# Optimization experiments

Hardware: AMD Instinct MI355X
Metric: run time of the kernel (lower is better)

The kernel has to match this reference:

```python
import jax, jax.numpy as jnp
import numpy as np

HEAD_DIM = 64
N_HEADS = 12
N_KV_HEADS = 4
N_REP = N_HEADS // N_KV_HEADS  # 3


def _rope(x, cos, sin):
    # x: [B, S, H, D]; cos/sin: [1, S, D//2] -> broadcast over heads
    x2 = x.reshape(*x.shape[:-1], -1, 2)          # [B,S,H,D/2,2]
    x_r, x_i = x2[..., 0], x2[..., 1]
    c = cos[:, :, None, :]                         # [1,S,1,D/2]
    s = sin[:, :, None, :]
    o_r = x_r * c - x_i * s
    o_i = x_r * s + x_i * c
    return jnp.stack([o_r, o_i], axis=-1).reshape(x.shape)


def setup_inputs() -> dict:
    key = jax.random.key(0)
    ks = jax.random.split(key, 6)
    B, S, H = 4, 2048, 768
    hidden_state = jax.random.normal(ks[0], (B, S, H), dtype=jnp.float32)
    # true RoPE frequencies (theta=10000) for positions 0..S-1
    inv_freq = 1.0 / (10000.0 ** (np.arange(0, HEAD_DIM, 2, dtype=np.float32) / HEAD_DIM))
    ang = np.arange(S, dtype=np.float32)[:, None] * inv_freq[None, :]  # [S, D/2]
    freqs_cos = jnp.asarray(np.cos(ang))[None]     # [1,S,32]
    freqs_sin = jnp.asarray(np.sin(ang))[None]
    sc = 0.02
    wq = jax.random.normal(ks[1], (768, 768), dtype=jnp.float32) * sc
    wk = jax.random.normal(ks[2], (256, 768), dtype=jnp.float32) * sc
    wv = jax.random.normal(ks[3], (256, 768), dtype=jnp.float32) * sc
    wo = jax.random.normal(ks[4], (768, 768), dtype=jnp.float32) * sc
    return {"hidden_state": hidden_state, "freqs_cos": freqs_cos, "freqs_sin": freqs_sin,
            "wq": wq, "wk": wk, "wv": wv, "wo": wo}


def reference(hidden_state, freqs_cos, freqs_sin, wq, wk, wv, wo):
    B, S, _ = hidden_state.shape
    q = (hidden_state @ wq.T).reshape(B, S, N_HEADS, HEAD_DIM)
    k = (hidden_state @ wk.T).reshape(B, S, N_KV_HEADS, HEAD_DIM)
    v = (hidden_state @ wv.T).reshape(B, S, N_KV_HEADS, HEAD_DIM)
    q = _rope(q, freqs_cos, freqs_sin)
    k = _rope(k, freqs_cos, freqs_sin)
    # repeat_kv: [B,S,KV,D] -> [B,S,KV*n_rep,D]
    k = jnp.repeat(k, N_REP, axis=2)
    v = jnp.repeat(v, N_REP, axis=2)
    q = q.transpose(0, 2, 1, 3)  # [B,H,S,D]
    k = k.transpose(0, 2, 1, 3)
    v = v.transpose(0, 2, 1, 3)
    scores = jnp.einsum('bhqd,bhkd->bhqk', q, k) / np.sqrt(HEAD_DIM).astype(np.float32)
    mask = jnp.triu(jnp.full((S, S), -jnp.inf, dtype=scores.dtype), k=1)
    scores = scores + mask
    attn = jax.nn.softmax(scores.astype(jnp.float32), axis=-1).astype(q.dtype)
    # dropout is inference-off (identity)
    out = jnp.einsum('bhqk,bhkd->bhqd', attn, v)
    out = out.transpose(0, 2, 1, 3).reshape(B, S, N_HEADS * HEAD_DIM)
    return out @ wo.T, attn
```

## Files before the change

kernel.cpp:

```cpp
#include <hip/hip_runtime.h>
#include <hip/hip_bf16.h>
#include <stdint.h>


typedef __bf16 bf16x8 __attribute__((ext_vector_type(8)));
typedef float  f32x4  __attribute__((ext_vector_type(4)));

#define B_    4
#define S_    2048
#define H_    768
#define NH_Q  12
#define NKV_  4
#define D_    64
#define MROWS (B_ * S_)
#define NQKV  1280
#define TILE_E (128 * 32)

__device__ __forceinline__ f32x4 mfma16(bf16x8 a, bf16x8 b, f32x4 c) {
  return __builtin_amdgcn_mfma_f32_16x16x32_bf16(a, b, c, 0, 0, 0);
}

__device__ __forceinline__ void st_nt4(float* p, f32x4 v) {
  __builtin_nontemporal_store(v, (f32x4*)p);
}

__device__ __forceinline__ uint32_t pk2(float a, float b) {
  __bf16 x = (__bf16)a, y = (__bf16)b;
  uint16_t xu = __builtin_bit_cast(uint16_t, x);
  uint16_t yu = __builtin_bit_cast(uint16_t, y);
  return (uint32_t)xu | ((uint32_t)yu << 16);
}
__device__ __forceinline__ float bl(uint32_t u) {
  uint32_t t = u << 16; return __builtin_bit_cast(float, t);
}
__device__ __forceinline__ float bh(uint32_t u) {
  uint32_t t = u & 0xffff0000u; return __builtin_bit_cast(float, t);
}

__device__ __forceinline__ void gload_lds16(const __bf16* g, __bf16* l) {
  __builtin_amdgcn_global_load_lds(
      (const __attribute__((address_space(1))) void*)g,
      (__attribute__((address_space(3))) void*)l, 16, 0, 0);
}

__global__ void cast_all(const float* __restrict__ X, const float* __restrict__ wq,
                         const float* __restrict__ wo, const float* __restrict__ wk,
                         const float* __restrict__ wv,
                         __bf16* __restrict__ Xb, __bf16* __restrict__ wqb,
                         __bf16* __restrict__ wob, __bf16* __restrict__ wkb,
                         __bf16* __restrict__ wvb) {
  int i = blockIdx.x * 256 + threadIdx.x;
  const int nX = MROWS * 768 / 8;
  const int nW = 768 * 768 / 8;
  const int nK = 256 * 768 / 8;
  const float* s; __bf16* d; int off;
  if (i < nX)                    { s = X;  d = Xb;  off = i; }
  else if (i < nX + nW)          { s = wq; d = wqb; off = i - nX; }
  else if (i < nX + 2 * nW)      { s = wo; d = wob; off = i - nX - nW; }
  else if (i < nX + 2 * nW + nK) { s = wk; d = wkb; off = i - nX - 2 * nW; }
  else if (i < nX + 2 * nW + 2 * nK) { s = wv; d = wvb; off = i - nX - 2 * nW - nK; }
  else return;
  const float4* sp = (const float4*)s + (size_t)off * 2;
  float4 a = sp[0], b = sp[1];
  bf16x8 o;
  o[0] = (__bf16)a.x; o[1] = (__bf16)a.y; o[2] = (__bf16)a.z; o[3] = (__bf16)a.w;
  o[4] = (__bf16)b.x; o[5] = (__bf16)b.y; o[6] = (__bf16)b.z; o[7] = (__bf16)b.w;
  *((bf16x8*)d + off) = o;
}

struct GemmPtrs {
  const __bf16 *gA0, *gA1, *gB0, *gB1;
};

__device__ __forceinline__ GemmPtrs make_ptrs(const __bf16* A, const __bf16* W,
                                              int m0, int n0, int K, int tid) {
  GemmPtrs gp;
  int c0 = tid, c1 = 256 + tid;
  int sr0 = c0 >> 2, kc0 = (c0 & 3) ^ ((sr0 >> 1) & 3);
  int sr1 = c1 >> 2, kc1 = (c1 & 3) ^ ((sr1 >> 1) & 3);
  gp.gA0 = A + (size_t)(m0 + sr0) * K + kc0 * 8;
  gp.gA1 = A + (size_t)(m0 + sr1) * K + kc1 * 8;
  gp.gB0 = W + (size_t)(n0 + sr0) * K + kc0 * 8;
  gp.gB1 = W + (size_t)(n0 + sr1) * K + kc1 * 8;
  return gp;
}

__device__ __forceinline__ void gemm_stage(GemmPtrs gp, int k0,
                                           __bf16* As, __bf16* Bs, int tid) {
  __bf16* lA0 = As + (size_t)(tid & ~63) * 8;
  __bf16* lB0 = Bs + (size_t)(tid & ~63) * 8;
  gload_lds16(gp.gA0 + k0, lA0);
  gload_lds16(gp.gA1 + k0, lA0 + 256 * 8);
  gload_lds16(gp.gB0 + k0, lB0);
  gload_lds16(gp.gB1 + k0, lB0 + 256 * 8);
}

__device__ __forceinline__ void gemm_core(GemmPtrs gp, int K,
                                          __bf16* As, __bf16* Bs,
                                          int tid, f32x4 (*acc)[4]) {
  const int lane = tid & 63, w = tid >> 6;
  const int wm = w >> 1, wn = w & 1;
  const int ql = lane & 15, grp = lane >> 4;

  gemm_stage(gp, 0, As, Bs, tid);
  __syncthreads();

  const int nk = K / 32;
  for (int ks = 0; ks < nk; ks++) {
    __bf16* curA = As + (ks & 1) * TILE_E;
    __bf16* curB = Bs + (ks & 1) * TILE_E;
    if (ks + 1 < nk)
      gemm_stage(gp, (ks + 1) * 32, As + ((ks + 1) & 1) * TILE_E,
                 Bs + ((ks + 1) & 1) * TILE_E, tid);

    bf16x8 af[4], bf_[4];
#pragma unroll
    for (int i = 0; i < 4; i++) {
      int row = wm * 64 + i * 16 + ql;
      int kc = grp ^ ((row >> 1) & 3);
      af[i] = *(const bf16x8*)(curA + row * 32 + kc * 8);
    }
#pragma unroll
    for (int j = 0; j < 4; j++) {
      int row = wn * 64 + j * 16 + ql;
      int kc = grp ^ ((row >> 1) & 3);
      bf_[j] = *(const bf16x8*)(curB + row * 32 + kc * 8);
    }
#pragma unroll
    for (int i = 0; i < 4; i++)
#pragma unroll
      for (int j = 0; j < 4; j++)
        acc[i][j] = mfma16(af[i], bf_[j], acc[i][j]);
    __syncthreads();
  }
}

__device__ __forceinline__ void gemm_store(f32x4 (*acc)[4], float* C, int N,
                                           int m0, int n0, int tid) {
  const int lane = tid & 63, w = tid >> 6;
  const int wm = w >> 1, wn = w & 1;
  const int ql = lane & 15, grp = lane >> 4;
#pragma unroll
  for (int i = 0; i < 4; i++)
#pragma unroll
    for (int j = 0; j < 4; j++)
#pragma unroll
      for (int r = 0; r < 4; r++) {
        int row = m0 + wm * 64 + i * 16 + grp * 4 + r;
        int col = n0 + wn * 64 + j * 16 + ql;
        C[(size_t)row * N + col] = acc[i][j][r];
      }
}

__global__ __launch_bounds__(256) void gemm_qkv(const __bf16* __restrict__ A,
                                                const __bf16* __restrict__ Wq,
                                                const __bf16* __restrict__ Wk,
                                                const __bf16* __restrict__ Wv,
                                                float* __restrict__ C) {
  __shared__ __bf16 As[2 * TILE_E];
  __shared__ __bf16 Bs[2 * TILE_E];
  const int m0 = blockIdx.x * 128, n0 = blockIdx.y * 128;
  const __bf16* W;
  int nl;
  if (n0 < 768)       { W = Wq; nl = n0; }
  else if (n0 < 1024) { W = Wk; nl = n0 - 768; }
  else                { W = Wv; nl = n0 - 1024; }
  const int tid = threadIdx.x;
  f32x4 acc[4][4] = {};
  GemmPtrs gp = make_ptrs(A, W, m0, nl, 768, tid);
  gemm_core(gp, 768, As, Bs, tid, acc);
  gemm_store(acc, C, NQKV, m0, n0, tid);
}

__global__ __launch_bounds__(256) void gemm_xwT(const __bf16* __restrict__ A,
                                                const __bf16* __restrict__ W,
                                                float* __restrict__ C,
                                                int M, int N, int K) {
  __shared__ __bf16 As[2 * TILE_E];
  __shared__ __bf16 Bs[2 * TILE_E];
  const int m0 = blockIdx.x * 128, n0 = blockIdx.y * 128;
  const int tid = threadIdx.x;
  f32x4 acc[4][4] = {};
  GemmPtrs gp = make_ptrs(A, W, m0, n0, K, tid);
  gemm_core(gp, K, As, Bs, tid, acc);
  gemm_store(acc, C, N, m0, n0, tid);
}

__global__ void rope_both(const float* __restrict__ QKV, const float* __restrict__ fc,
                          const float* __restrict__ fs, __bf16* __restrict__ Qb,
                          __bf16* __restrict__ Kb) {
  int idx = blockIdx.x * 256 + threadIdx.x;
  const int NQp = MROWS * NH_Q * 32;
  int NH, colOff;
  __bf16* dst;
  float scale;
  if (idx < NQp) {
    NH = NH_Q; colOff = 0; dst = Qb; scale = 0.125f * 1.44269504f;
  } else {
    idx -= NQp;
    NH = NKV_; colOff = 768; dst = Kb; scale = 1.0f;
  }
  int t = idx & 31;
  int h = (idx >> 5) % NH;
  int row = idx / (32 * NH);
  int s = row & (S_ - 1), b = row >> 11;
  float x0 = QKV[(size_t)row * NQKV + colOff + h * 64 + 2 * t];
  float x1 = QKV[(size_t)row * NQKV + colOff + h * 64 + 2 * t + 1];
  float c = fc[s * 32 + t], sn = fs[s * 32 + t];
  float o0 = (x0 * c - x1 * sn) * scale;
  float o1 = (x0 * sn + x1 * c) * scale;
  __bf16* d = dst + (((size_t)(b * NH + h) * S_ + s) * 64 + 2 * t);
  d[0] = (__bf16)o0;
  d[1] = (__bf16)o1;
}

__global__ void transpose_v(const float* __restrict__ QKV, __bf16* __restrict__ VT) {
  __shared__ float tile[64][65];
  int rt = blockIdx.x;
  int ct = blockIdx.y;
  int r0 = rt * 64, c0 = ct * 64;
  int tx = threadIdx.x & 63, ty = threadIdx.x >> 6;
#pragma unroll
  for (int rep = 0; rep < 16; rep++) {
    int rr = rep * 4 + ty;
    tile[rr][tx] = QKV[(size_t)(r0 + rr) * NQKV + 1024 + c0 + tx];
  }
  __syncthreads();
  int b = r0 >> 11;
  int s0 = r0 & (S_ - 1);
#pragma unroll
  for (int rep = 0; rep < 16; rep++) {
    int dr = rep * 4 + ty;
    int d = c0 + dr;
    int kv = d >> 6, dd = d & 63;
    VT[(((size_t)(b * NKV_ + kv) * 64 + dd) * S_) + s0 + tx] = (__bf16)tile[tx][dr];
  }
}

template <int MAXC>
__device__ __forceinline__ void attn_part(
    int g, int b, int h, int w, int lane,
    const __bf16* __restrict__ Q, const __bf16* __restrict__ Kp,
    const __bf16* __restrict__ Vp, float* __restrict__ attn,
    __bf16* __restrict__ O, float (*lsum_s)[16], f32x4 (*obuf)[4]) {
  const int ql = lane & 15, grp = lane >> 4;
  const int qr0 = g * 16;
  const int nch = (g >> 1) + 1;
  const int i_q = qr0 + ql;
  const __bf16* Qp = Q + ((size_t)(b * NH_Q + h) * S_ + qr0) * 64;
  float* attnp = attn + ((size_t)(b * NH_Q + h) * S_ + qr0) * S_;

  bf16x8 bq0 = *(const bf16x8*)(Qp + ql * 64 + grp * 8);
  bf16x8 bq1 = *(const bf16x8*)(Qp + ql * 64 + 32 + grp * 8);

  uint32_t p[MAXC][4];
  float lsum = 0.f;

#pragma unroll
  for (int c = 0; c < MAXC; c++) {
    const int j = w + 4 * c;
    if (j < nch) {
      const int j0 = j * 32;
      bf16x8 k0 = *(const bf16x8*)(Kp + (size_t)(j0 + ql) * 64 + grp * 8);
      bf16x8 k1 = *(const bf16x8*)(Kp + (size_t)(j0 + ql) * 64 + 32 + grp * 8);
      bf16x8 k2 = *(const bf16x8*)(Kp + (size_t)(j0 + 16 + ql) * 64 + grp * 8);
      bf16x8 k3 = *(const bf16x8*)(Kp + (size_t)(j0 + 16 + ql) * 64 + 32 + grp * 8);
      f32x4 s0 = {}, s1 = {};
      s0 = mfma16(k0, bq0, s0);
      s0 = mfma16(k1, bq1, s0);
      s1 = mfma16(k2, bq0, s1);
      s1 = mfma16(k3, bq1, s1);
      float e[8];
      if (j == nch - 1) {
#pragma unroll
        for (int r = 0; r < 4; r++) {
          int ja = j0 + grp * 4 + r, jb = j0 + 16 + grp * 4 + r;
          e[r]     = (ja <= i_q) ? exp2f(s0[r]) : 0.f;
          e[4 + r] = (jb <= i_q) ? exp2f(s1[r]) : 0.f;
        }
      } else {
#pragma unroll
        for (int r = 0; r < 4; r++) {
          e[r]     = exp2f(s0[r]);
          e[4 + r] = exp2f(s1[r]);
        }
      }
#pragma unroll
      for (int r = 0; r < 8; r++) lsum += e[r];
      p[c][0] = pk2(e[0], e[1]);
      p[c][1] = pk2(e[2], e[3]);
      p[c][2] = pk2(e[4], e[5]);
      p[c][3] = pk2(e[6], e[7]);
    }
  }

  lsum += __shfl_xor(lsum, 16);
  lsum += __shfl_xor(lsum, 32);
  if (lane < 16) lsum_s[w][ql] = lsum;
  __syncthreads();
  const float rinv = 1.f / (lsum_s[0][ql] + lsum_s[1][ql] + lsum_s[2][ql] + lsum_s[3][ql]);

  f32x4 opv[4] = {};
#pragma unroll
  for (int c = 0; c < MAXC; c++) {
    const int j = w + 4 * c;
    if (j < nch) {
      const int j0 = j * 32;
      bf16x8 v0 = *(const bf16x8*)(Vp + (size_t)(0 * 16 + ql) * S_ + j0 + grp * 8);
      bf16x8 v1 = *(const bf16x8*)(Vp + (size_t)(1 * 16 + ql) * S_ + j0 + grp * 8);
      bf16x8 v2 = *(const bf16x8*)(Vp + (size_t)(2 * 16 + ql) * S_ + j0 + grp * 8);
      bf16x8 v3 = *(const bf16x8*)(Vp + (size_t)(3 * 16 + ql) * S_ + j0 + grp * 8);

      f32x4 q0, q1;
      q0[0] = bl(p[c][0]); q0[1] = bh(p[c][0]); q0[2] = bl(p[c][1]); q0[3] = bh(p[c][1]);
      q1[0] = bl(p[c][2]); q1[1] = bh(p[c][2]); q1[2] = bl(p[c][3]); q1[3] = bh(p[c][3]);
#pragma unroll
      for (int r = 0; r < 4; r++) { q0[r] *= rinv; q1[r] *= rinv; }
      st_nt4(attnp + (size_t)ql * S_ + j0 + grp * 4, q0);
      st_nt4(attnp + (size_t)ql * S_ + j0 + 16 + grp * 4, q1);

      int srcA = ql + 32 * (grp & 1);
      int srcB = srcA + 16;
      uint32_t A0 = __shfl(p[c][0], srcA), A1 = __shfl(p[c][1], srcA);
      uint32_t A2 = __shfl(p[c][2], srcA), A3 = __shfl(p[c][3], srcA);
      uint32_t B0 = __shfl(p[c][0], srcB), B1 = __shfl(p[c][1], srcB);
      uint32_t B2 = __shfl(p[c][2], srcB), B3 = __shfl(p[c][3], srcB);
      bool hi = (grp >> 1) != 0;
      union { bf16x8 v; uint32_t u[4]; } pu;
      pu.u[0] = hi ? A2 : A0;
      pu.u[1] = hi ? A3 : A1;
      pu.u[2] = hi ? B2 : B0;
      pu.u[3] = hi ? B3 : B1;
      opv[0] = mfma16(pu.v, v0, opv[0]);
      opv[1] = mfma16(pu.v, v1, opv[1]);
      opv[2] = mfma16(pu.v, v2, opv[2]);
      opv[3] = mfma16(pu.v, v3, opv[3]);
    }
  }

  f32x4* ob = obuf[w * 64 + lane];
  ob[0] = opv[0]; ob[1] = opv[1]; ob[2] = opv[2]; ob[3] = opv[3];
  __syncthreads();
  {
    const int dt = w;
    f32x4 acc = obuf[0 * 64 + lane][dt];
    acc += obuf[1 * 64 + lane][dt];
    acc += obuf[2 * 64 + lane][dt];
    acc += obuf[3 * 64 + lane][dt];
    __bf16* Op = O + ((size_t)(b * S_) + qr0) * H_ + h * 64;
#pragma unroll
    for (int r = 0; r < 4; r++) {
      int row = grp * 4 + r;
      float rr = 1.f / (lsum_s[0][row] + lsum_s[1][row] + lsum_s[2][row] + lsum_s[3][row]);
      Op[(size_t)row * H_ + dt * 16 + ql] = (__bf16)(acc[r] * rr);
    }
  }

  const int jz = nch * 32;
  const int tid = w * 64 + lane;
  const f32x4 z4 = {0.f, 0.f, 0.f, 0.f};
#pragma unroll 1
  for (int rr = 0; rr < 16; rr++) {
    float* rowp = attnp + (size_t)rr * S_;
    for (int jj = jz + tid * 4; jj < S_; jj += 1024) st_nt4(rowp + jj, z4);
  }
  __syncthreads();
}

__global__ __launch_bounds__(256) void attn_kernel(const __bf16* __restrict__ Q,
                                                   const __bf16* __restrict__ Kb,
                                                   const __bf16* __restrict__ VT,
                                                   float* __restrict__ attn,
                                                   __bf16* __restrict__ O) {
  __shared__ float lsum_s[4][16];
  __shared__ f32x4 obuf[4 * 64][4];
  const int bid = blockIdx.x;
  const int r = bid & 7;
  const int qd = bid >> 3;
  const int x = qd & 63;
  const int idx6 = qd >> 6;
  const int g48 = idx6 * 8 + r;
  const int h = g48 >> 2, b = g48 & 3;
  const int lane = threadIdx.x & 63, w = threadIdx.x >> 6;
  const int kv = h / 3;
  const __bf16* Kp = Kb + (size_t)(b * NKV_ + kv) * S_ * 64;
  const __bf16* Vp = VT + (size_t)(b * NKV_ + kv) * 64 * S_;

  attn_part<8>(x, b, h, w, lane, Q, Kp, Vp, attn, O, lsum_s, obuf);
  attn_part<16>(127 - x, b, h, w, lane, Q, Kp, Vp, attn, O, lsum_s, obuf);
}

extern "C" void kernel_launch(void* const* d_in, const int* in_sizes, int n_in,
                              void* d_out, int out_size, void* d_ws, size_t ws_size,
                              hipStream_t stream) {
  (void)in_sizes; (void)n_in;
  const float* X  = (const float*)d_in[0];
  const float* fc = (const float*)d_in[1];
  const float* fs = (const float*)d_in[2];
  const float* wq = (const float*)d_in[3];
  const float* wk = (const float*)d_in[4];
  const float* wv = (const float*)d_in[5];
  const float* wo = (const float*)d_in[6];
  float* out0 = (float*)d_out;
  float* attn = out0 + (size_t)B_ * S_ * H_;

  char* p = (char*)d_ws;
  auto take = [&](size_t bytes) -> char* {
    char* r = p;
    p += (bytes + 255) & ~(size_t)255;
    return r;
  };
  __bf16* wqbf = (__bf16*)take((size_t)768 * 768 * 2);
  __bf16* wkbf = (__bf16*)take((size_t)256 * 768 * 2);
  __bf16* wvbf = (__bf16*)take((size_t)256 * 768 * 2);
  __bf16* wobf = (__bf16*)take((size_t)768 * 768 * 2);
  __bf16* Qbf  = (__bf16*)take((size_t)MROWS * 768 * 2);
  __bf16* Kbf  = (__bf16*)take((size_t)MROWS * 256 * 2);
  __bf16* VTbf = (__bf16*)take((size_t)MROWS * 256 * 2);
  __bf16* Obf  = (__bf16*)take((size_t)MROWS * 768 * 2);
  size_t used = (size_t)(p - (char*)d_ws);

  const size_t XBF_B  = (size_t)MROWS * 768 * 2;
  const size_t QKV_B  = (size_t)MROWS * NQKV * 4;
  const size_t TEMP_B = XBF_B + QKV_B;

  char* tp;
  if (used + TEMP_B + 1024 <= ws_size) {
    tp = p;
  } else {
    tp = (char*)(((uintptr_t)((char*)d_out + (size_t)out_size * 4 - TEMP_B)) & ~(uintptr_t)255);
  }
  __bf16* Xbf  = (__bf16*)tp;  tp += XBF_B;
  float*  QKVf = (float*)tp;

  {
    const int total8 = MROWS * 768 / 8 + 2 * (768 * 768 / 8) + 2 * (256 * 768 / 8);
    cast_all<<<(total8 + 255) / 256, 256, 0, stream>>>(X, wq, wo, wk, wv,
                                                       Xbf, wqbf, wobf, wkbf, wvbf);
  }

  gemm_qkv<<<dim3(MROWS / 128, NQKV / 128), 256, 0, stream>>>(Xbf, wqbf, wkbf, wvbf, QKVf);

  {
    const int totalPairs = MROWS * NH_Q * 32 + MROWS * NKV_ * 32;
    rope_both<<<(totalPairs + 255) / 256, 256, 0, stream>>>(QKVf, fc, fs, Qbf, Kbf);
  }
  transpose_v<<<dim3(MROWS / 64, 4), 256, 0, stream>>>(QKVf, VTbf);

  attn_kernel<<<dim3(48 * 64), 256, 0, stream>>>(Qbf, Kbf, VTbf, attn, Obf);

  gemm_xwT<<<dim3(MROWS / 128, 768 / 128), 256, 0, stream>>>(Obf, wobf, out0, MROWS, 768, 768);
}
```

Before: 292.7 us.

## Fuse RoPE and bf16 conversion into QKV GEMM epilogue

The QKV projection GEMM now applies RoPE (pairing even/odd columns through a lane shuffle) and writes bf16 Q/K directly in head-major layout, and writes V as a bf16 row-major buffer. The separate rope kernel and the fp32 QKV intermediate are removed, which eliminates one launch and a large fp32 write/read round trip. The transpose of V now reads bf16. The cost is an epilogue with scattered 2-byte stores and per-element cos/sin loads inside the GEMM.

```diff
diff --git a/kernel.cpp b/kernel.cpp
--- a/kernel.cpp
+++ b/kernel.cpp
@@ -156,7 +156,11 @@
                                                 const __bf16* __restrict__ Wq,
                                                 const __bf16* __restrict__ Wk,
                                                 const __bf16* __restrict__ Wv,
-                                                float* __restrict__ C) {
+                                                const float* __restrict__ fc,
+                                                const float* __restrict__ fs,
+                                                __bf16* __restrict__ Qb,
+                                                __bf16* __restrict__ Kb,
+                                                __bf16* __restrict__ Vrow) {
   __shared__ __bf16 As[2 * TILE_E];
   __shared__ __bf16 Bs[2 * TILE_E];
   const int m0 = blockIdx.x * 128, n0 = blockIdx.y * 128;
@@ -169,7 +173,47 @@
   f32x4 acc[4][4] = {};
   GemmPtrs gp = make_ptrs(A, W, m0, nl, 768, tid);
   gemm_core(gp, 768, As, Bs, tid, acc);
-  gemm_store(acc, C, NQKV, m0, n0, tid);
+
+  const int lane = tid & 63, w = tid >> 6;
+  const int wm = w >> 1, wn = w & 1;
+  const int ql = lane & 15, grp = lane >> 4;
+
+  if (n0 < 1024) {
+    __bf16* dst; int NH, hbase; float scale;
+    if (n0 < 768) { dst = Qb; NH = NH_Q; hbase = 0;   scale = 0.125f * 1.44269504f; }
+    else          { dst = Kb; NH = NKV_; hbase = 768; scale = 1.0f; }
+#pragma unroll
+    for (int i = 0; i < 4; i++)
+#pragma unroll
+      for (int j = 0; j < 4; j++) {
+        const int col = n0 + wn * 64 + j * 16 + ql;
+        const int hd = col - hbase;
+        const int h = hd >> 6, d = hd & 63, t = d >> 1;
+        const bool ev = (d & 1) == 0;
+#pragma unroll
+        for (int r = 0; r < 4; r++) {
+          const int row = m0 + wm * 64 + i * 16 + grp * 4 + r;
+          const int s = row & (S_ - 1), b = row >> 11;
+          float x = acc[i][j][r];
+          float xo = __shfl_xor(x, 1);
+          float c = fc[s * 32 + t], sn = fs[s * 32 + t];
+          float o = ev ? (x * c - xo * sn) : (xo * sn + x * c);
+          dst[(((size_t)(b * NH + h) * S_ + s) << 6) + d] = (__bf16)(o * scale);
+        }
+      }
+  } else {
+#pragma unroll
+    for (int i = 0; i < 4; i++)
+#pragma unroll
+      for (int j = 0; j < 4; j++) {
+        const int colv = n0 - 1024 + wn * 64 + j * 16 + ql;
+#pragma unroll
+        for (int r = 0; r < 4; r++) {
+          const int row = m0 + wm * 64 + i * 16 + grp * 4 + r;
+          Vrow[(size_t)row * 256 + colv] = (__bf16)acc[i][j][r];
+        }
+      }
+  }
 }
 
 __global__ __launch_bounds__(256) void gemm_xwT(const __bf16* __restrict__ A,
@@ -186,35 +230,7 @@
   gemm_store(acc, C, N, m0, n0, tid);
 }
 
-__global__ void rope_both(const float* __restrict__ QKV, const float* __restrict__ fc,
-                          const float* __restrict__ fs, __bf16* __restrict__ Qb,
-                          __bf16* __restrict__ Kb) {
-  int idx = blockIdx.x * 256 + threadIdx.x;
-  const int NQp = MROWS * NH_Q * 32;
-  int NH, colOff;
-  __bf16* dst;
-  float scale;
-  if (idx < NQp) {
-    NH = NH_Q; colOff = 0; dst = Qb; scale = 0.125f * 1.44269504f;
-  } else {
-    idx -= NQp;
-    NH = NKV_; colOff = 768; dst = Kb; scale = 1.0f;
-  }
-  int t = idx & 31;
-  int h = (idx >> 5) % NH;
-  int row = idx / (32 * NH);
-  int s = row & (S_ - 1), b = row >> 11;
-  float x0 = QKV[(size_t)row * NQKV + colOff + h * 64 + 2 * t];
-  float x1 = QKV[(size_t)row * NQKV + colOff + h * 64 + 2 * t + 1];
-  float c = fc[s * 32 + t], sn = fs[s * 32 + t];
-  float o0 = (x0 * c - x1 * sn) * scale;
-  float o1 = (x0 * sn + x1 * c) * scale;
-  __bf16* d = dst + (((size_t)(b * NH + h) * S_ + s) * 64 + 2 * t);
-  d[0] = (__bf16)o0;
-  d[1] = (__bf16)o1;
-}
-
-__global__ void transpose_v(const float* __restrict__ QKV, __bf16* __restrict__ VT) {
+__global__ void transpose_v(const __bf16* __restrict__ Vrow, __bf16* __restrict__ VT) {
   __shared__ float tile[64][65];
   int rt = blockIdx.x;
   int ct = blockIdx.y;
@@ -223,7 +239,7 @@
 #pragma unroll
   for (int rep = 0; rep < 16; rep++) {
     int rr = rep * 4 + ty;
-    tile[rr][tx] = QKV[(size_t)(r0 + rr) * NQKV + 1024 + c0 + tx];
+    tile[rr][tx] = (float)Vrow[(size_t)(r0 + rr) * 256 + c0 + tx];
   }
   __syncthreads();
   int b = r0 >> 11;
@@ -421,8 +437,8 @@
   size_t used = (size_t)(p - (char*)d_ws);
 
   const size_t XBF_B  = (size_t)MROWS * 768 * 2;
-  const size_t QKV_B  = (size_t)MROWS * NQKV * 4;
-  const size_t TEMP_B = XBF_B + QKV_B;
+  const size_t VROW_B = (size_t)MROWS * 256 * 2;
+  const size_t TEMP_B = XBF_B + VROW_B;
 
   char* tp;
   if (used + TEMP_B + 1024 <= ws_size) {
@@ -431,7 +447,7 @@
     tp = (char*)(((uintptr_t)((char*)d_out + (size_t)out_size * 4 - TEMP_B)) & ~(uintptr_t)255);
   }
   __bf16* Xbf  = (__bf16*)tp;  tp += XBF_B;
-  float*  QKVf = (float*)tp;
+  __bf16* Vrow = (__bf16*)tp;
 
   {
     const int total8 = MROWS * 768 / 8 + 2 * (768 * 768 / 8) + 2 * (256 * 768 / 8);
@@ -439,13 +455,10 @@
                                                        Xbf, wqbf, wobf, wkbf, wvbf);
   }
 
-  gemm_qkv<<<dim3(MROWS / 128, NQKV / 128), 256, 0, stream>>>(Xbf, wqbf, wkbf, wvbf, QKVf);
-
-  {
-    const int totalPairs = MROWS * NH_Q * 32 + MROWS * NKV_ * 32;
-    rope_both<<<(totalPairs + 255) / 256, 256, 0, stream>>>(QKVf, fc, fs, Qbf, Kbf);
-  }
-  transpose_v<<<dim3(MROWS / 64, 4), 256, 0, stream>>>(QKVf, VTbf);
+  gemm_qkv<<<dim3(MROWS / 128, NQKV / 128), 256, 0, stream>>>(
+      Xbf, wqbf, wkbf, wvbf, fc, fs, Qbf, Kbf, Vrow);
+
+  transpose_v<<<dim3(MROWS / 64, 4), 256, 0, stream>>>(Vrow, VTbf);
 
   attn_kernel<<<dim3(48 * 64), 256, 0, stream>>>(Qbf, Kbf, VTbf, attn, Obf);
 
```

New measurement: 299.2 us. 1.02x slower.
